# Kernel tuning notes

Measured on AMD Instinct MI355X. Metric: run time of the kernel, lower is better.

The kernel has to match this reference:

```python
import jax, jax.numpy as jnp
import numpy as np


def setup_inputs() -> dict:
    key = jax.random.key(0)
    kq, kk, kv = jax.random.split(key, 3)
    B, Hq, Hkv, S, D = 2, 32, 8, 2048, 128
    q = jax.random.normal(kq, (B, Hq, S, D), dtype=jnp.float32)
    k = jax.random.normal(kk, (B, Hkv, S, D), dtype=jnp.float32)
    v = jax.random.normal(kv, (B, Hkv, S, D), dtype=jnp.float32)
    return {"q": q, "k": k, "v": v}


def reference(q, k, v):
    # GQA: q heads are grouped; repeat_interleave(group, dim=1) on k/v is
    # equivalent to reshaping q's head dim into (Hkv, group) blocks.
    B, Hq, S, D = q.shape
    Hkv = k.shape[1]
    g = Hq // Hkv
    qg = q.reshape(B, Hkv, g, S, D)  # [b, hkv, g, s, d]
    scale = (1.0 / D) ** 0.5
    scores = jnp.einsum('bhgsd,bhkd->bhgsk', qg, k) * scale  # [b,hkv,g,s,k]
    probs = jax.nn.softmax(scores, axis=-1)
    o = jnp.einsum('bhgsk,bhkd->bhgsd', probs, v)
    return o.reshape(B, Hq, S, D).astype(jnp.float16)
```

## Files before the change

### kernel.cpp

```cpp
#include <hip/hip_runtime.h>
#include <hip/hip_fp16.h>

typedef _Float16 f16;
typedef _Float16 f16x2 __attribute__((ext_vector_type(2)));
typedef _Float16 f16x8 __attribute__((ext_vector_type(8)));
typedef __fp16 h16x2 __attribute__((ext_vector_type(2)));
typedef float f32x4 __attribute__((ext_vector_type(4)));
typedef float f32x16 __attribute__((ext_vector_type(16)));

#define EXP2F(x) __builtin_amdgcn_exp2f(x)

__device__ __forceinline__ f16x2 pk2(float a, float b) {
  h16x2 t = __builtin_amdgcn_cvt_pkrtz(a, b);
  return __builtin_bit_cast(f16x2, t);
}

union U8 { f16x8 v; f16x2 h[4]; };

namespace {
constexpr int D  = 128;
constexpr int S  = 2048;
constexpr int BM = 256;
constexpr int BN = 64;
constexpr int NT = S / BN;
constexpr int NH = 16;
constexpr size_t TILE_B = 16384;
constexpr size_t IMG_B  = (size_t)NH * NT * TILE_B;
constexpr float QSCALE = 0.08838834764831845f * 1.4426950408889634f;
__device__ __forceinline__ int sig(int c) {
  return (c & ~12) | ((c & 4) << 1) | ((c & 8) >> 1);
}
}

__device__ __forceinline__ f16* kptr(char* s, int buf, int key, int g) {
  return (f16*)(s + buf * 16384 + key * 256 + ((g ^ (key & 7)) << 4));
}
__device__ __forceinline__ f16* vptr(char* s, int buf, int d, int g) {
  return (f16*)(s + 65536 + buf * 16384 + d * 128 + ((g ^ (d & 7)) << 4));
}

__global__ __launch_bounds__(512) void convert_kv(
    const float* __restrict__ Kg, const float* __restrict__ Vg,
    char* __restrict__ Kimg, char* __restrict__ Vimg) {
  const int blk = blockIdx.x;
  const int hd = blk >> 5, t = blk & 31;
  const int tid = threadIdx.x;

  if (tid < 256) {
    const float* Ks = Kg + ((size_t)hd * S + (size_t)t * BN) * D;
    char* Kd = Kimg + ((size_t)hd * NT + t) * TILE_B;
    const int r = tid >> 2, gs = tid & 3;
    const float* row = Ks + (size_t)r * D;
#pragma unroll
    for (int j = 0; j < 4; ++j) {
      const int g = 4 * gs + j;
      f32x4 a = *(const f32x4*)(row + g * 8);
      f32x4 c = *(const f32x4*)(row + g * 8 + 4);
      U8 u;
      u.h[0] = pk2(a[0], a[1]); u.h[1] = pk2(a[2], a[3]);
      u.h[2] = pk2(c[0], c[1]); u.h[3] = pk2(c[2], c[3]);
      *(f16x8*)(Kd + r * 256 + ((g ^ (r & 7)) << 4)) = u.v;
    }
  } else {
    const float* Vs = Vg + ((size_t)hd * S + (size_t)t * BN) * D;
    char* Vd = Vimg + ((size_t)hd * NT + t) * TILE_B;
    const int s = tid - 256;
    const int vg = s & 7, vd4 = s >> 3;
    const int R0 = (vg >> 1) * 16 + (vg & 1) * 4;
    f32x4 st[8];
#pragma unroll
    for (int e = 0; e < 4; ++e) {
      st[e]     = *(const f32x4*)(Vs + (size_t)(R0 + e) * D + vd4 * 4);
      st[4 + e] = *(const f32x4*)(Vs + (size_t)(R0 + 8 + e) * D + vd4 * 4);
    }
#pragma unroll
    for (int j = 0; j < 4; ++j) {
      const int d = vd4 * 4 + j;
      const int pv = vg ^ (d & 7);
      U8 u;
      u.h[0] = pk2(st[0][j], st[1][j]);
      u.h[1] = pk2(st[2][j], st[3][j]);
      u.h[2] = pk2(st[4][j], st[5][j]);
      u.h[3] = pk2(st[6][j], st[7][j]);
      *(f16x8*)(Vd + d * 128 + pv * 16) = u.v;
    }
  }
}

__global__ __launch_bounds__(512, 2) void fa_fwd(
    const float* __restrict__ Qg, float* __restrict__ Og,
    const char* __restrict__ Kimg, const char* __restrict__ Vimg) {
  __shared__ __align__(16) char smem[131072];

  const int tid  = threadIdx.x;
  const int lane = tid & 63;
  const int warp = tid >> 6;
  const int l31  = lane & 31;
  const int h    = lane >> 5;

  const int bid = blockIdx.x;
  const int qt  = bid >> 6;
  const int bh  = bid & 63;
  const int hq  = bh & 31;
  const int b   = bh >> 5;
  const int hkv = hq >> 2;
  const int hd  = b * 8 + hkv;

  const float* Qb = Qg + ((size_t)bh * S + (size_t)qt * BM) * D;
  float* Ob = Og + ((size_t)bh * S + (size_t)qt * BM) * D;

  f16x8 qf[8];
  {
    const float* qrow = Qb + (size_t)(warp * 32 + l31) * D;
#pragma unroll
    for (int kc = 0; kc < 8; ++kc) {
      f32x4 a = *(const f32x4*)(qrow + kc * 16 + h * 8);
      f32x4 c = *(const f32x4*)(qrow + kc * 16 + h * 8 + 4);
      U8 u;
      u.h[0] = pk2(a[0] * QSCALE, a[1] * QSCALE);
      u.h[1] = pk2(a[2] * QSCALE, a[3] * QSCALE);
      u.h[2] = pk2(c[0] * QSCALE, c[1] * QSCALE);
      u.h[3] = pk2(c[2] * QSCALE, c[3] * QSCALE);
      qf[kc] = u.v;
    }
  }

  const bool kw = warp < 4;
  const int rgn = (kw ? warp : warp - 4) * 4096 + lane * 16;
  const char* gs0 = (kw ? Kimg : Vimg) + (size_t)hd * (NT * TILE_B) + rgn;
  const int lds0 = (kw ? 0 : 65536) + rgn;

  f16x8 st16[4];
  auto stage_load = [&](int tt) {
    const char* s = gs0 + (size_t)tt * TILE_B;
#pragma unroll
    for (int i = 0; i < 4; ++i) st16[i] = *(const f16x8*)(s + i * 1024);
  };
  auto stage_write = [&](int buf) {
    char* l = smem + buf * 16384 + lds0;
#pragma unroll
    for (int i = 0; i < 4; ++i) *(f16x8*)(l + i * 1024) = st16[i];
  };

  f32x16 o_acc[4];
#pragma unroll
  for (int dt = 0; dt < 4; ++dt)
#pragma unroll
    for (int r = 0; r < 16; ++r) o_acc[dt][r] = 0.f;
  float l_acc = 0.f;

  stage_load(0); stage_write(0);
  stage_load(1); stage_write(1);
  __syncthreads();

  auto halfiter = [&](int tt) {
    const int q = tt & 3;
    if (tt + 2 < NT) stage_load(tt + 2);

    f32x16 sc0, sc1;
#pragma unroll
    for (int r = 0; r < 16; ++r) { sc0[r] = 0.f; sc1[r] = 0.f; }
    __builtin_amdgcn_s_setprio(1);
#pragma unroll
    for (int kc = 0; kc < 8; ++kc) {
      f16x8 kf0 = *(const f16x8*)kptr(smem, q, l31, kc * 2 + h);
      f16x8 kf1 = *(const f16x8*)kptr(smem, q, 32 + l31, kc * 2 + h);
      sc0 = __builtin_amdgcn_mfma_f32_32x32x16_f16(kf0, qf[kc], sc0, 0, 0, 0);
      sc1 = __builtin_amdgcn_mfma_f32_32x32x16_f16(kf1, qf[kc], sc1, 0, 0, 0);
    }
    __builtin_amdgcn_s_setprio(0);

    float lsum = 0.f;
#pragma unroll
    for (int r = 0; r < 16; ++r) {
      float p0 = EXP2F(sc0[r]);
      float p1 = EXP2F(sc1[r]);
      sc0[r] = p0; sc1[r] = p1;
      lsum += p0 + p1;
    }
    lsum += __shfl_xor(lsum, 32, 64);
    l_acc += lsum;

    f16x8 pf[4];
    {
      U8 u0, u1, u2, u3;
#pragma unroll
      for (int i = 0; i < 4; ++i) {
        u0.h[i] = pk2(sc0[2 * i], sc0[2 * i + 1]);
        u1.h[i] = pk2(sc0[8 + 2 * i], sc0[9 + 2 * i]);
        u2.h[i] = pk2(sc1[2 * i], sc1[2 * i + 1]);
        u3.h[i] = pk2(sc1[8 + 2 * i], sc1[9 + 2 * i]);
      }
      pf[0] = u0.v; pf[1] = u1.v; pf[2] = u2.v; pf[3] = u3.v;
    }

    if (tt + 2 < NT) stage_write((tt + 2) & 3);

    __builtin_amdgcn_s_setprio(1);
#pragma unroll
    for (int kcp = 0; kcp < 4; ++kcp)
#pragma unroll
      for (int dt = 0; dt < 4; ++dt) {
        f16x8 vf = *(const f16x8*)vptr(smem, q, dt * 32 + l31, kcp * 2 + h);
        o_acc[dt] = __builtin_amdgcn_mfma_f32_32x32x16_f16(vf, pf[kcp], o_acc[dt], 0, 0, 0);
      }
    __builtin_amdgcn_s_setprio(0);
  };

  for (int t = 0; t < NT; t += 2) {
    halfiter(t);
    halfiter(t + 1);
    __syncthreads();
  }

  const float inv = 1.0f / l_acc;
  float* wreg = (float*)smem + warp * 1088;
#pragma unroll
  for (int pass = 0; pass < 4; ++pass) {
    __syncthreads();
    if ((l31 >> 3) == pass) {
      float* rowp = wreg + (l31 & 7) * 136;
#pragma unroll
      for (int dt = 0; dt < 4; ++dt)
#pragma unroll
        for (int k = 0; k < 4; ++k) {
          f32x4 v;
#pragma unroll
          for (int e = 0; e < 4; ++e) v[e] = o_acc[dt][4 * k + e] * inv;
          *(f32x4*)(rowp + dt * 32 + 8 * k + 4 * h) = v;
        }
    }
    __syncthreads();
    {
      const int r = lane >> 3, c = lane & 7;
      const float* rowp = wreg + r * 136;
      float* og = Ob + (size_t)(warp * 32 + pass * 8 + r) * D;
#pragma unroll
      for (int i = 0; i < 4; ++i)
        *(f32x4*)(og + i * 32 + c * 4) = *(const f32x4*)(rowp + i * 32 + c * 4);
    }
  }
}

__global__ __launch_bounds__(512, 2) void fa_fwd8(
    const float* __restrict__ Qg, const float* __restrict__ Kg,
    const float* __restrict__ Vg, float* __restrict__ Og) {
  __shared__ __align__(16) char smem[65536];
  constexpr int BN8 = 64, NT8 = 32;

  const int tid  = threadIdx.x;
  const int lane = tid & 63;
  const int warp = tid >> 6;
  const int l31  = lane & 31;
  const int h    = lane >> 5;

  const int bid = blockIdx.x;
  const int qt  = bid & 7;
  const int bh  = bid >> 3;
  const int hq  = bh & 31;
  const int b   = bh >> 5;
  const int hkv = hq >> 2;
  const int hd  = b * 8 + hkv;

  const float* Qb = Qg + ((size_t)bh * S + (size_t)qt * BM) * D;
  const float* Kb = Kg + ((size_t)hd * S) * D;
  const float* Vb = Vg + ((size_t)hd * S) * D;
  float* Ob = Og + ((size_t)bh * S + (size_t)qt * BM) * D;

  auto kp = [&](int buf, int key, int g) -> f16* {
    return (f16*)(smem + buf * 16384 + key * 256 + ((g ^ (key & 7)) << 4));
  };
  auto vp = [&](int buf, int d, int g) -> f16* {
    return (f16*)(smem + 32768 + buf * 16384 + d * 128 + ((g ^ (d & 7)) << 4));
  };

  f16x8 qf[8];
  {
    const float* qrow = Qb + (size_t)(warp * 32 + l31) * D;
#pragma unroll
    for (int kc = 0; kc < 8; ++kc) {
      f32x4 a = *(const f32x4*)(qrow + kc * 16 + h * 8);
      f32x4 c = *(const f32x4*)(qrow + kc * 16 + h * 8 + 4);
      U8 u;
      u.h[0] = pk2(a[0] * QSCALE, a[1] * QSCALE);
      u.h[1] = pk2(a[2] * QSCALE, a[3] * QSCALE);
      u.h[2] = pk2(c[0] * QSCALE, c[1] * QSCALE);
      u.h[3] = pk2(c[2] * QSCALE, c[3] * QSCALE);
      qf[kc] = u.v;
    }
  }

  const bool kw = warp < 4;
  const int st   = kw ? tid : tid - 256;
  const int skey = st >> 2;
  const int ka   = st & 3;
  const int vkg  = st & 7;
  const int vd4  = st >> 3;

  const float* pA;
  const float* pB;
  if (kw) {
    pA = Kb + (size_t)skey * D + ka * 32;
    pB = pA;
  } else {
    const int R0 = (vkg >> 1) * 16 + (vkg & 1) * 4;
    pA = Vb + (size_t)R0 * D + vd4 * 4;
    pB = pA + 8 * (size_t)D;
  }

  f32x16 o_acc[4];
#pragma unroll
  for (int dt = 0; dt < 4; ++dt)
#pragma unroll
    for (int r = 0; r < 16; ++r) o_acc[dt][r] = 0.f;
  float l_acc = 0.f;

  f32x4 stg[8];
  f16x8 st16[4];

  auto prefetch = [&]() {
    if (kw) {
#pragma unroll
      for (int i = 0; i < 8; ++i) stg[i] = *(const f32x4*)(pA + 4 * i);
    } else {
#pragma unroll
      for (int i = 0; i < 4; ++i) {
        stg[i]     = *(const f32x4*)(pA + (size_t)i * D);
        stg[4 + i] = *(const f32x4*)(pB + (size_t)i * D);
      }
    }
    pA += BN8 * D;
    pB += BN8 * D;
  };
  auto convert = [&]() {
    if (kw) {
#pragma unroll
      for (int j = 0; j < 4; ++j) {
        U8 u;
        u.h[0] = pk2(stg[2 * j][0], stg[2 * j][1]);
        u.h[1] = pk2(stg[2 * j][2], stg[2 * j][3]);
        u.h[2] = pk2(stg[2 * j + 1][0], stg[2 * j + 1][1]);
        u.h[3] = pk2(stg[2 * j + 1][2], stg[2 * j + 1][3]);
        st16[j] = u.v;
      }
    } else {
#pragma unroll
      for (int r = 0; r < 4; ++r) {
        U8 u;
        u.h[0] = pk2(stg[0][r], stg[1][r]);
        u.h[1] = pk2(stg[2][r], stg[3][r]);
        u.h[2] = pk2(stg[4][r], stg[5][r]);
        u.h[3] = pk2(stg[6][r], stg[7][r]);
        st16[r] = u.v;
      }
    }
  };
  auto lds_write = [&](int buf) {
    if (kw) {
#pragma unroll
      for (int j = 0; j < 4; ++j)
        *(f16x8*)kp(buf, skey, 4 * ka + j) = st16[j];
    } else {
#pragma unroll
      for (int r = 0; r < 4; ++r)
        *(f16x8*)vp(buf, vd4 * 4 + r, vkg) = st16[r];
    }
  };

  prefetch();
  convert();
  lds_write(0);
  __syncthreads();

  for (int t = 0; t < NT8; ++t) {
    const int p = t & 1;
    if (t + 1 < NT8) prefetch();

    f32x16 sc0, sc1;
#pragma unroll
    for (int r = 0; r < 16; ++r) { sc0[r] = 0.f; sc1[r] = 0.f; }
    __builtin_amdgcn_s_setprio(1);
#pragma unroll
    for (int kc = 0; kc < 8; ++kc) {
      f16x8 kf0 = *(const f16x8*)kp(p, l31, kc * 2 + h);
      f16x8 kf1 = *(const f16x8*)kp(p, 32 + l31, kc * 2 + h);
      sc0 = __builtin_amdgcn_mfma_f32_32x32x16_f16(kf0, qf[kc], sc0, 0, 0, 0);
      sc1 = __builtin_amdgcn_mfma_f32_32x32x16_f16(kf1, qf[kc], sc1, 0, 0, 0);
    }
    __builtin_amdgcn_s_setprio(0);

    float lsum = 0.f;
#pragma unroll
    for (int r = 0; r < 16; ++r) {
      float p0 = EXP2F(sc0[r]);
      float p1 = EXP2F(sc1[r]);
      sc0[r] = p0; sc1[r] = p1;
      lsum += p0 + p1;
    }
    lsum += __shfl_xor(lsum, 32, 64);
    l_acc += lsum;

    f16x8 pf[4];
    {
      U8 u0, u1, u2, u3;
#pragma unroll
      for (int i = 0; i < 4; ++i) {
        u0.h[i] = pk2(sc0[2 * i], sc0[2 * i + 1]);
        u1.h[i] = pk2(sc0[8 + 2 * i], sc0[9 + 2 * i]);
        u2.h[i] = pk2(sc1[2 * i], sc1[2 * i + 1]);
        u3.h[i] = pk2(sc1[8 + 2 * i], sc1[9 + 2 * i]);
      }
      pf[0] = u0.v; pf[1] = u1.v; pf[2] = u2.v; pf[3] = u3.v;
    }

    if (t + 1 < NT8) {
      convert();
      lds_write(p ^ 1);
    }

    __builtin_amdgcn_s_setprio(1);
#pragma unroll
    for (int kcp = 0; kcp < 4; ++kcp)
#pragma unroll
      for (int dt = 0; dt < 4; ++dt) {
        f16x8 vf = *(const f16x8*)vp(p, dt * 32 + l31, kcp * 2 + h);
        o_acc[dt] = __builtin_amdgcn_mfma_f32_32x32x16_f16(vf, pf[kcp], o_acc[dt], 0, 0, 0);
      }
    __builtin_amdgcn_s_setprio(0);

    __syncthreads();
  }

  const float inv = 1.0f / l_acc;
  float* wreg = (float*)smem + warp * 1088;
#pragma unroll
  for (int pass = 0; pass < 4; ++pass) {
    __syncthreads();
    if ((l31 >> 3) == pass) {
      float* rowp = wreg + (l31 & 7) * 136;
#pragma unroll
      for (int dt = 0; dt < 4; ++dt)
#pragma unroll
        for (int k = 0; k < 4; ++k) {
          f32x4 v;
#pragma unroll
          for (int e = 0; e < 4; ++e) v[e] = o_acc[dt][4 * k + e] * inv;
          *(f32x4*)(rowp + dt * 32 + 8 * k + 4 * h) = v;
        }
    }
    __syncthreads();
    {
      const int r = lane >> 3, c = lane & 7;
      const float* rowp = wreg + r * 136;
      float* og = Ob + (size_t)(warp * 32 + pass * 8 + r) * D;
#pragma unroll
      for (int i = 0; i < 4; ++i)
        *(f32x4*)(og + i * 32 + c * 4) = *(const f32x4*)(rowp + i * 32 + c * 4);
    }
  }
}

extern "C" void kernel_launch(void* const* d_in, const int* in_sizes, int n_in,
                              void* d_out, int out_size, void* d_ws, size_t ws_size,
                              hipStream_t stream) {
  const float* q = (const float*)d_in[0];
  const float* k = (const float*)d_in[1];
  const float* v = (const float*)d_in[2];
  float* out = (float*)d_out;
  const bool pre = d_ws && ws_size >= 2 * IMG_B;
  if (pre) {
    char* Kimg = (char*)d_ws;
    char* Vimg = Kimg + IMG_B;
    convert_kv<<<dim3(NH * NT), dim3(512), 0, stream>>>(k, v, Kimg, Vimg);
    fa_fwd<<<dim3(64 * (S / BM)), dim3(512), 0, stream>>>(q, out, Kimg, Vimg);
  } else {
    fa_fwd8<<<dim3(64 * (S / BM)), dim3(512), 0, stream>>>(q, k, v, out);
  }
}
```

Before: 270.5 us.

## Software-pipeline QK of next tile ahead of softmax and PV of current tile

Replaces the two sequential half-iterations with a manually pipelined body. The second tile's QK^T MFMAs are issued before the first tile's exp/pack and PV, so the softmax VALU work can overlap with matrix work. The next tile's global stage load/write is interleaved at new points. This keeps both score accumulators live at once, which raises register pressure and could lower occupancy or cause spills.

```diff
diff --git a/kernel.cpp b/kernel.cpp
--- a/kernel.cpp
+++ b/kernel.cpp
@@ -153,63 +153,107 @@
   stage_load(1); stage_write(1);
   __syncthreads();
 
-  auto halfiter = [&](int tt) {
-    const int q = tt & 3;
-    if (tt + 2 < NT) stage_load(tt + 2);
-
-    f32x16 sc0, sc1;
-#pragma unroll
-    for (int r = 0; r < 16; ++r) { sc0[r] = 0.f; sc1[r] = 0.f; }
+  for (int t = 0; t < NT; t += 2) {
+    const int q0 = t & 3, q1 = (t + 1) & 3;
+
+    if (t + 2 < NT) stage_load(t + 2);
+
+    f32x16 sa0, sa1;
+#pragma unroll
+    for (int r = 0; r < 16; ++r) { sa0[r] = 0.f; sa1[r] = 0.f; }
     __builtin_amdgcn_s_setprio(1);
 #pragma unroll
     for (int kc = 0; kc < 8; ++kc) {
-      f16x8 kf0 = *(const f16x8*)kptr(smem, q, l31, kc * 2 + h);
-      f16x8 kf1 = *(const f16x8*)kptr(smem, q, 32 + l31, kc * 2 + h);
-      sc0 = __builtin_amdgcn_mfma_f32_32x32x16_f16(kf0, qf[kc], sc0, 0, 0, 0);
-      sc1 = __builtin_amdgcn_mfma_f32_32x32x16_f16(kf1, qf[kc], sc1, 0, 0, 0);
+      f16x8 kf0 = *(const f16x8*)kptr(smem, q0, l31, kc * 2 + h);
+      f16x8 kf1 = *(const f16x8*)kptr(smem, q0, 32 + l31, kc * 2 + h);
+      sa0 = __builtin_amdgcn_mfma_f32_32x32x16_f16(kf0, qf[kc], sa0, 0, 0, 0);
+      sa1 = __builtin_amdgcn_mfma_f32_32x32x16_f16(kf1, qf[kc], sa1, 0, 0, 0);
     }
     __builtin_amdgcn_s_setprio(0);
 
+    if (t + 2 < NT) stage_write((t + 2) & 3);
+
+    f32x16 sb0, sb1;
+#pragma unroll
+    for (int r = 0; r < 16; ++r) { sb0[r] = 0.f; sb1[r] = 0.f; }
+    __builtin_amdgcn_s_setprio(1);
+#pragma unroll
+    for (int kc = 0; kc < 8; ++kc) {
+      f16x8 kf0 = *(const f16x8*)kptr(smem, q1, l31, kc * 2 + h);
+      f16x8 kf1 = *(const f16x8*)kptr(smem, q1, 32 + l31, kc * 2 + h);
+      sb0 = __builtin_amdgcn_mfma_f32_32x32x16_f16(kf0, qf[kc], sb0, 0, 0, 0);
+      sb1 = __builtin_amdgcn_mfma_f32_32x32x16_f16(kf1, qf[kc], sb1, 0, 0, 0);
+    }
+    __builtin_amdgcn_s_setprio(0);
+
     float lsum = 0.f;
 #pragma unroll
     for (int r = 0; r < 16; ++r) {
-      float p0 = EXP2F(sc0[r]);
-      float p1 = EXP2F(sc1[r]);
-      sc0[r] = p0; sc1[r] = p1;
+      float p0 = EXP2F(sa0[r]);
+      float p1 = EXP2F(sa1[r]);
+      sa0[r] = p0; sa1[r] = p1;
       lsum += p0 + p1;
     }
+    f16x8 pfa[4];
+    {
+      U8 u0, u1, u2, u3;
+#pragma unroll
+      for (int i = 0; i < 4; ++i) {
+        u0.h[i] = pk2(sa0[2 * i], sa0[2 * i + 1]);
+        u1.h[i] = pk2(sa0[8 + 2 * i], sa0[9 + 2 * i]);
+        u2.h[i] = pk2(sa1[2 * i], sa1[2 * i + 1]);
+        u3.h[i] = pk2(sa1[8 + 2 * i], sa1[9 + 2 * i]);
+      }
+      pfa[0] = u0.v; pfa[1] = u1.v; pfa[2] = u2.v; pfa[3] = u3.v;
+    }
+
+    __builtin_amdgcn_s_setprio(1);
+#pragma unroll
+    for (int kcp = 0; kcp < 4; ++kcp)
+#pragma unroll
+      for (int dt = 0; dt < 4; ++dt) {
+        f16x8 vf = *(const f16x8*)vptr(smem, q0, dt * 32 + l31, kcp * 2 + h);
+        o_acc[dt] = __builtin_amdgcn_mfma_f32_32x32x16_f16(vf, pfa[kcp], o_acc[dt], 0, 0, 0);
+      }
+    __builtin_amdgcn_s_setprio(0);
+
+    if (t + 3 < NT) stage_load(t + 3);
+
+#pragma unroll
+    for (int r = 0; r < 16; ++r) {
+      float p0 = EXP2F(sb0[r]);
+      float p1 = EXP2F(sb1[r]);
+      sb0[r] = p0; sb1[r] = p1;
+      lsum += p0 + p1;
+    }
+    f16x8 pfb[4];
+    {
+      U8 u0, u1, u2, u3;
+#pragma unroll
+      for (int i = 0; i < 4; ++i) {
+        u0.h[i] = pk2(sb0[2 * i], sb0[2 * i + 1]);
+        u1.h[i] = pk2(sb0[8 + 2 * i], sb0[9 + 2 * i]);
+        u2.h[i] = pk2(sb1[2 * i], sb1[2 * i + 1]);
+        u3.h[i] = pk2(sb1[8 + 2 * i], sb1[9 + 2 * i]);
+      }
+      pfb[0] = u0.v; pfb[1] = u1.v; pfb[2] = u2.v; pfb[3] = u3.v;
+    }
+
     lsum += __shfl_xor(lsum, 32, 64);
     l_acc += lsum;
 
-    f16x8 pf[4];
-    {
-      U8 u0, u1, u2, u3;
-#pragma unroll
-      for (int i = 0; i < 4; ++i) {
-        u0.h[i] = pk2(sc0[2 * i], sc0[2 * i + 1]);
-        u1.h[i] = pk2(sc0[8 + 2 * i], sc0[9 + 2 * i]);
-        u2.h[i] = pk2(sc1[2 * i], sc1[2 * i + 1]);
-        u3.h[i] = pk2(sc1[8 + 2 * i], sc1[9 + 2 * i]);
-      }
-      pf[0] = u0.v; pf[1] = u1.v; pf[2] = u2.v; pf[3] = u3.v;
-    }
-
-    if (tt + 2 < NT) stage_write((tt + 2) & 3);
+    if (t + 3 < NT) stage_write((t + 3) & 3);
 
     __builtin_amdgcn_s_setprio(1);
 #pragma unroll
     for (int kcp = 0; kcp < 4; ++kcp)
 #pragma unroll
       for (int dt = 0; dt < 4; ++dt) {
-        f16x8 vf = *(const f16x8*)vptr(smem, q, dt * 32 + l31, kcp * 2 + h);
-        o_acc[dt] = __builtin_amdgcn_mfma_f32_32x32x16_f16(vf, pf[kcp], o_acc[dt], 0, 0, 0);
+        f16x8 vf = *(const f16x8*)vptr(smem, q1, dt * 32 + l31, kcp * 2 + h);
+        o_acc[dt] = __builtin_amdgcn_mfma_f32_32x32x16_f16(vf, pfb[kcp], o_acc[dt], 0, 0, 0);
       }
     __builtin_amdgcn_s_setprio(0);
-  };
-
-  for (int t = 0; t < NT; t += 2) {
-    halfiter(t);
-    halfiter(t + 1);
+
     __syncthreads();
   }
 
```

Measured after the change: 270.6 us. Within noise of the previous version (+0.1%).
